# Optimization experiments

Measured on AMD Instinct MI355X. Metric: run time of the kernel, lower is better.

Reference implementation:

```python
import jax, jax.numpy as jnp
import numpy as np

B, C, H, W = 64, 64, 56, 56
MID = 2 * C  # two output nodes concatenated
EPS = 1e-5


def _conv1x1(x, w):
    # x: [B,C,H,W], w: [O,C] (1x1 conv kernel squeezed)
    return jnp.einsum('bchw,oc->bohw', x, w)


def _bn(x, g, b, m, v):
    # eval-mode BatchNorm2d with running stats
    sc = g * jax.lax.rsqrt(v + EPS)
    return x * sc[None, :, None, None] + (b - m * sc)[None, :, None, None]


def _maxpool3(x):
    # MaxPool2d(kernel=3, stride=1, padding=1)
    return jax.lax.reduce_window(x, -jnp.inf, jax.lax.max,
                                 (1, 1, 3, 3), (1, 1, 1, 1),
                                 [(0, 0), (0, 0), (1, 1), (1, 1)])


def _avgpool3(x):
    # AvgPool2d(kernel=3, stride=1, padding=1), count_include_pad=True -> /9
    s = jax.lax.reduce_window(x, 0.0, jax.lax.add,
                              (1, 1, 3, 3), (1, 1, 1, 1),
                              [(0, 0), (0, 0), (1, 1), (1, 1)])
    return s * (1.0 / 9.0)


def setup_inputs() -> dict:
    key = jax.random.key(0)
    ks = jax.random.split(key, 11)
    x = jax.random.normal(ks[0], (B, C, H, W), dtype=jnp.float32)
    w1 = jax.random.normal(ks[1], (C, C), dtype=jnp.float32) * 0.1
    w2 = jax.random.normal(ks[2], (C, MID), dtype=jnp.float32) * 0.1
    bn1_g = 1.0 + 0.1 * jax.random.normal(ks[3], (C,), dtype=jnp.float32)
    bn1_b = 0.1 * jax.random.normal(ks[4], (C,), dtype=jnp.float32)
    bn1_m = 0.1 * jax.random.normal(ks[5], (C,), dtype=jnp.float32)
    bn1_v = jax.random.uniform(ks[6], (C,), minval=0.5, maxval=1.5, dtype=jnp.float32)
    bn2_g = 1.0 + 0.1 * jax.random.normal(ks[7], (C,), dtype=jnp.float32)
    bn2_b = 0.1 * jax.random.normal(ks[8], (C,), dtype=jnp.float32)
    bn2_m = 0.1 * jax.random.normal(ks[9], (C,), dtype=jnp.float32)
    bn2_v = jax.random.uniform(ks[10], (C,), minval=0.5, maxval=1.5, dtype=jnp.float32)
    return dict(x=x, w1=w1, w2=w2,
                bn1_g=bn1_g, bn1_b=bn1_b, bn1_m=bn1_m, bn1_v=bn1_v,
                bn2_g=bn2_g, bn2_b=bn2_b, bn2_m=bn2_m, bn2_v=bn2_v)


def reference(x, w1, w2, bn1_g, bn1_b, bn1_m, bn1_v, bn2_g, bn2_b, bn2_m, bn2_v):
    # DAG g = [[[0,1],[1,2]], [[4,3],[3]], [[5,3],[3,100]], [[4,3],[100]]]
    # topoSort order: [0, 2, 1, 3]; output nodes (ordered): [2, 3]
    node0 = jax.nn.relu(_bn(_conv1x1(x, w1), bn1_g, bn1_b, bn1_m, bn1_v))
    node1 = _maxpool3(node0)            # op type 4, pred {0}
    node2 = _avgpool3(node0)            # op type 5, pred {0}
    node3 = _maxpool3(node1) + _maxpool3(node2)  # op type 4, preds {1,2}, summed
    cat = jnp.concatenate([node2, node3], axis=1)  # [B, 2C, H, W]
    out = jax.nn.relu(_bn(_conv1x1(cat, w2), bn2_g, bn2_b, bn2_m, bn2_v))
    return out
```

## Files before the change

kernel.cpp:

```cpp
#include <hip/hip_runtime.h>
#include <cstddef>

#define EPS 1e-5f
static constexpr int Bn = 64, Cn = 64, Hn = 56, Wn = 56, HWn = Hn * Wn;
static constexpr int XS = 65;
static constexpr int RB = 8;
static constexpr int NBAND = 7;
static constexpr int SLAB = 3600;

typedef __attribute__((ext_vector_type(8))) short short8;
typedef __attribute__((ext_vector_type(8))) unsigned short ushort8;
typedef __attribute__((ext_vector_type(4))) unsigned short ushort4v;
typedef __attribute__((ext_vector_type(4))) float floatx4;
typedef __attribute__((ext_vector_type(4))) unsigned int uintx4;
typedef __attribute__((ext_vector_type(2))) unsigned int uintx2;

__device__ __forceinline__ unsigned pack_rne(float a, float b) {
    unsigned ua = __float_as_uint(a), ub = __float_as_uint(b);
    ua = ua + 0x7fffu + ((ua >> 16) & 1u);
    ub = ub + 0x7fffu + ((ub >> 16) & 1u);
    return __builtin_amdgcn_perm(ub, ua, 0x07060302);
}
__device__ __forceinline__ unsigned pack_trunc(float a, float b) {
    return __builtin_amdgcn_perm(__float_as_uint(b), __float_as_uint(a), 0x07060302);
}
__device__ __forceinline__ ushort8 pmax(ushort8 a, ushort8 b) {
    return __builtin_elementwise_max(a, b);
}
__device__ __forceinline__ uintx2 pmax2(uintx2 a, uintx2 b) {
    ushort4v r = __builtin_elementwise_max(*(ushort4v*)&a, *(ushort4v*)&b);
    return *(uintx2*)&r;
}
__device__ __forceinline__ float bf_lo(unsigned u) { return __uint_as_float(u << 16); }
__device__ __forceinline__ float bf_hi(unsigned u) { return __uint_as_float(u & 0xffff0000u); }


__global__ __launch_bounds__(256) void k1_conv1(
    const float* __restrict__ x, const float* __restrict__ w1,
    const float* __restrict__ bg, const float* __restrict__ bb,
    const float* __restrict__ bm, const float* __restrict__ bv,
    unsigned short* __restrict__ node0)
{
    __shared__ float xs[2][64 * XS];
    __shared__ float scs[64], shs[64];
    const int tid = threadIdx.x;
    if (tid < 64) {
        float sc = bg[tid] * rsqrtf(bv[tid] + EPS);
        scs[tid] = sc;
        shs[tid] = bb[tid] - bm[tid] * sc;
    }
    __syncthreads();
    const int lane = tid & 63;
    const int wv   = tid >> 6;
    const int m    = lane & 15;
    const int quad = lane >> 4;
    const int qoff = quad * 8;

    short8 afr[4][2];
    float shv[16];
    #pragma unroll
    for (int t = 0; t < 4; ++t) {
        const float sc = scs[t * 16 + m];
        #pragma unroll
        for (int kk = 0; kk < 2; ++kk) {
            const float* wp = w1 + (t * 16 + m) * 64 + kk * 32 + qoff;
            floatx4 f0 = *(const floatx4*)wp;
            floatx4 f1 = *(const floatx4*)(wp + 4);
            uintx4 u;
            u.x = pack_rne(f0[0] * sc, f0[1] * sc);
            u.y = pack_rne(f0[2] * sc, f0[3] * sc);
            u.z = pack_rne(f1[0] * sc, f1[1] * sc);
            u.w = pack_rne(f1[2] * sc, f1[3] * sc);
            afr[t][kk] = *(short8*)&u;
        }
        #pragma unroll
        for (int i = 0; i < 4; ++i) shv[t * 4 + i] = shs[t * 16 + quad * 4 + i];
    }

    floatx4 stg[4];
    auto ldtile = [&](int tt) {
        const int P = blockIdx.x * 256 + tt * 64;
        const int b = P / HWn, p0 = P - b * HWn;
        #pragma unroll
        for (int q = 0; q < 4; ++q) {
            int idx = q * 256 + tid;
            int c = idx >> 4, f = idx & 15;
            stg[q] = *(const floatx4*)(x + (size_t)(b * 64 + c) * HWn + p0 + f * 4);
        }
    };
    auto sttile = [&](int buf) {
        #pragma unroll
        for (int q = 0; q < 4; ++q) {
            int idx = q * 256 + tid;
            int c = idx >> 4, f = idx & 15;
            #pragma unroll
            for (int k = 0; k < 4; ++k)
                xs[buf][(f * 4 + k) * XS + c] = stg[q][k];
        }
    };

    ldtile(0);
    sttile(0);

    #pragma unroll
    for (int tt = 0; tt < 4; ++tt) {
        __syncthreads();
        if (tt < 3) ldtile(tt + 1);

        const int P = blockIdx.x * 256 + tt * 64;
        const int b = P / HWn, p0 = P - b * HWn;
        const float* xr = &xs[tt & 1][(wv * 16 + m) * XS];

        floatx4 acc[4];
        #pragma unroll
        for (int t = 0; t < 4; ++t) acc[t] = (floatx4){0.f, 0.f, 0.f, 0.f};

        #pragma unroll
        for (int kk = 0; kk < 2; ++kk) {
            float f[8];
            #pragma unroll
            for (int j = 0; j < 8; ++j) f[j] = xr[kk * 32 + qoff + j];
            uintx4 u;
            u.x = pack_trunc(f[0], f[1]);
            u.y = pack_trunc(f[2], f[3]);
            u.z = pack_trunc(f[4], f[5]);
            u.w = pack_trunc(f[6], f[7]);
            short8 bfr = *(short8*)&u;
            #pragma unroll
            for (int t = 0; t < 4; ++t)
                acc[t] = __builtin_amdgcn_mfma_f32_16x16x32_bf16(afr[t][kk], bfr, acc[t], 0, 0, 0);
        }

        const int chunkbase = (quad >> 1);
        const int j0 = (quad & 1) * 4;
        #pragma unroll
        for (int t = 0; t < 4; ++t) {
            float v0 = acc[t][0] + shv[t * 4 + 0]; v0 = v0 > 0.f ? v0 : 0.f;
            float v1 = acc[t][1] + shv[t * 4 + 1]; v1 = v1 > 0.f ? v1 : 0.f;
            float v2 = acc[t][2] + shv[t * 4 + 2]; v2 = v2 > 0.f ? v2 : 0.f;
            float v3 = acc[t][3] + shv[t * 4 + 3]; v3 = v3 > 0.f ? v3 : 0.f;
            uintx2 st;
            st.x = pack_rne(v0, v1);
            st.y = pack_rne(v2, v3);
            int chunk = t * 2 + chunkbase;
            *(uintx2*)(node0 + ((size_t)(b * 8 + chunk) * HWn + p0 + wv * 16 + m) * 8 + j0) = st;
        }

        if (tt < 3) sttile((tt + 1) & 1);
    }
}

__global__ __launch_bounds__(1024, 4) void k23_fused(
    const unsigned short* __restrict__ node0,
    const float* __restrict__ w2,
    const float* __restrict__ bg, const float* __restrict__ bb,
    const float* __restrict__ bm, const float* __restrict__ bv,
    float* __restrict__ out)
{
    __shared__ __align__(16) unsigned short catl[16 * SLAB];
    const int tid = threadIdx.x;
    const int lane = tid & 63;
    const int wv = tid >> 6;

    const int bid = blockIdx.x;
    const int xcd = bid & 7;
    const int jj = bid >> 3;
    const int b = xcd * 8 + jj / NBAND;
    const int band = jj % NBAND;
    const int lo = band * RB;

    {
        const int chunk = wv >> 1;
        const int c0 = (wv & 1) * 28;
        const int local = lane >> 1;
        const int col = c0 - 2 + local;
        const int jh = lane & 1;
        const unsigned short* base = node0 + ((size_t)(b * 8 + chunk) * HWn) * 8 + jh * 4;

        const uintx2 zz = (uintx2){0u, 0u};
        auto loadrow = [&](int r) -> uintx2 {
            if (((unsigned)col >= (unsigned)Wn) | ((unsigned)r >= (unsigned)Hn)) return zz;
            return *(const uintx2*)(base + (size_t)(r * Wn + col) * 8);
        };

        float hs1[4], hs2[4];
        #pragma unroll
        for (int c = 0; c < 4; ++c) hs1[c] = hs2[c] = 0.f;
        uintx2 h5a = zz, h5b = zz, h5c = zz, h5d = zz, nh1 = zz, nh2 = zz;

        uintx2 cur = loadrow(lo - 2);
        uintx2 nxt = loadrow(lo - 1);

        unsigned short* cav = catl + (size_t)(chunk * 2) * SLAB + jh * 4;
        unsigned short* cmx = cav + SLAB;
        const bool stcol = (local >= 2) & (local <= 29);

        #pragma unroll
        for (int i = 0; i < RB + 4; ++i) {
            const int r = lo - 2 + i;
            uintx2 nx2 = (i < RB + 2) ? loadrow(r + 2) : zz;

            uintx2 D0, D1, D3, D4;
            #pragma unroll
            for (int w = 0; w < 2; ++w) {
                unsigned u = cur[w];
                D1[w] = __shfl_up(u, 2);
                D0[w] = __shfl_up(u, 4);
                D3[w] = __shfl_down(u, 2);
                D4[w] = __shfl_down(u, 4);
            }

            uintx2 hm5 = pmax2(pmax2(pmax2(D0, D1), pmax2(cur, D3)), D4);
            uintx2 m5 = pmax2(pmax2(pmax2(h5a, h5b), pmax2(h5c, h5d)), hm5);
            h5a = h5b; h5b = h5c; h5c = h5d; h5d = hm5;

            float a2[4];
            #pragma unroll
            for (int w = 0; w < 2; ++w) {
                float s0 = bf_lo(D1[w]) + bf_lo(cur[w]) + bf_lo(D3[w]);
                float s1 = bf_hi(D1[w]) + bf_hi(cur[w]) + bf_hi(D3[w]);
                a2[w * 2 + 0] = (hs2[w * 2 + 0] + hs1[w * 2 + 0] + s0) * (1.f / 9.f);
                a2[w * 2 + 1] = (hs2[w * 2 + 1] + hs1[w * 2 + 1] + s1) * (1.f / 9.f);
                hs2[w * 2 + 0] = hs1[w * 2 + 0]; hs1[w * 2 + 0] = s0;
                hs2[w * 2 + 1] = hs1[w * 2 + 1]; hs1[w * 2 + 1] = s1;
            }
            uintx2 ap;
            ap.x = pack_rne(a2[0], a2[1]);
            ap.y = pack_rne(a2[2], a2[3]);

            uintx2 al, ar;
            #pragma unroll
            for (int w = 0; w < 2; ++w) {
                al[w] = __shfl_up(ap[w], 2);
                ar[w] = __shfl_down(ap[w], 2);
            }
            uintx2 nh = pmax2(pmax2(al, ap), ar);
            uintx2 m3 = pmax2(pmax2(nh2, nh1), nh);
            nh2 = nh1; nh1 = nh;

            const int r2 = r - 1, r3 = r - 2;
            if (stcol && i >= 3 && i <= RB + 2)
                *(uintx2*)(cav + (size_t)((r2 - lo) * Wn + col) * 8) = ap;
            if (stcol && i >= 4) {
                uintx2 st;
                st.x = pack_rne(bf_lo(m5.x) + bf_lo(m3.x), bf_hi(m5.x) + bf_hi(m3.x));
                st.y = pack_rne(bf_lo(m5.y) + bf_lo(m3.y), bf_hi(m5.y) + bf_hi(m3.y));
                *(uintx2*)(cmx + (size_t)((r3 - lo) * Wn + col) * 8) = st;
            }
            cur = nxt; nxt = nx2;
        }
    }

    const int m16 = lane & 15;
    const int q = lane >> 4;
    const int t = wv & 3;
    const int e = wv >> 2;
    short8 afr[4];
    #pragma unroll
    for (int cp = 0; cp < 4; ++cp) {
        const int c = 2 * cp + (q >> 1);
        const int chb = ((q & 1) ? 64 : 0) + 8 * c;
        const float* wp = w2 + (size_t)(t * 16 + m16) * 128 + chb;
        floatx4 f0 = *(const floatx4*)wp;
        floatx4 f1 = *(const floatx4*)(wp + 4);
        uintx4 u;
        u.x = pack_rne(f0[0], f0[1]);
        u.y = pack_rne(f0[2], f0[3]);
        u.z = pack_rne(f1[0], f1[1]);
        u.w = pack_rne(f1[2], f1[3]);
        afr[cp] = *(short8*)&u;
    }
    const int oc0 = t * 16 + q * 4;
    floatx4 g4 = *(const floatx4*)(bg + oc0);
    floatx4 bb4 = *(const floatx4*)(bb + oc0);
    floatx4 mm4 = *(const floatx4*)(bm + oc0);
    floatx4 vv4 = *(const floatx4*)(bv + oc0);
    float sc[4], sh[4];
    #pragma unroll
    for (int r = 0; r < 4; ++r) {
        sc[r] = g4[r] * rsqrtf(vv4[r] + EPS);
        sh[r] = bb4[r] - mm4[r] * sc[r];
    }
    __syncthreads();

    floatx4 acc[7];
    #pragma unroll
    for (int i = 0; i < 7; ++i) acc[i] = (floatx4){0.f, 0.f, 0.f, 0.f};

    #pragma unroll
    for (int cp = 0; cp < 4; ++cp) {
        #pragma unroll
        for (int i = 0; i < 7; ++i) {
            const int px = (e * 7 + i) * 16 + m16;
            short8 bfr = *(const short8*)(catl + (size_t)(4 * cp + q) * SLAB + (size_t)px * 8);
            acc[i] = __builtin_amdgcn_mfma_f32_16x16x32_bf16(afr[cp], bfr, acc[i], 0, 0, 0);
        }
    }

    float* ob = out + (size_t)(b * 64 + oc0) * HWn + lo * Wn;
    #pragma unroll
    for (int i = 0; i < 7; ++i) {
        const int px = (e * 7 + i) * 16 + m16;
        #pragma unroll
        for (int r = 0; r < 4; ++r) {
            float v = fmaf(acc[i][r], sc[r], sh[r]);
            ob[(size_t)r * HWn + px] = v > 0.f ? v : 0.f;
        }
    }
}

extern "C" void kernel_launch(void* const* d_in, const int* in_sizes, int n_in,
                              void* d_out, int out_size, void* d_ws, size_t ws_size,
                              hipStream_t stream)
{
    const float* x   = (const float*)d_in[0];
    const float* w1  = (const float*)d_in[1];
    const float* w2  = (const float*)d_in[2];
    const float* b1g = (const float*)d_in[3];
    const float* b1b = (const float*)d_in[4];
    const float* b1m = (const float*)d_in[5];
    const float* b1v = (const float*)d_in[6];
    const float* b2g = (const float*)d_in[7];
    const float* b2b = (const float*)d_in[8];
    const float* b2m = (const float*)d_in[9];
    const float* b2v = (const float*)d_in[10];

    float* out = (float*)d_out;
    unsigned short* node0 = (unsigned short*)d_ws;

    k1_conv1<<<dim3(784), dim3(256), 0, stream>>>(x, w1, b1g, b1b, b1m, b1v, node0);
    k23_fused<<<dim3(Bn * NBAND), dim3(1024), 0, stream>>>(node0, w2, b2g, b2b, b2m, b2v, out);
}
```

Before: 146.6 us.

## Rewrite conv1 with 32x32x16 MFMA and direct global loads, drop LDS staging

The first 1x1 conv kernel no longer stages a transposed x tile through shared memory with double buffering. Each wave now loads its 32 pixels x 64 channels straight from global memory into registers and runs 32x32x16 bf16 MFMAs for two 32-channel output halves. Launch bounds now request 4 blocks per CU. This removes the LDS writes and reads and the per-tile barriers, but the global loads become strided per channel: each lane reads one float per channel row, coalesced across lanes only within a 32-pixel span.

```diff
diff --git a/kernel.cpp b/kernel.cpp
--- a/kernel.cpp
+++ b/kernel.cpp
@@ -3,7 +3,6 @@
 
 #define EPS 1e-5f
 static constexpr int Bn = 64, Cn = 64, Hn = 56, Wn = 56, HWn = Hn * Wn;
-static constexpr int XS = 65;
 static constexpr int RB = 8;
 static constexpr int NBAND = 7;
 static constexpr int SLAB = 3600;
@@ -12,6 +11,7 @@
 typedef __attribute__((ext_vector_type(8))) unsigned short ushort8;
 typedef __attribute__((ext_vector_type(4))) unsigned short ushort4v;
 typedef __attribute__((ext_vector_type(4))) float floatx4;
+typedef __attribute__((ext_vector_type(16))) float floatx16;
 typedef __attribute__((ext_vector_type(4))) unsigned int uintx4;
 typedef __attribute__((ext_vector_type(2))) unsigned int uintx2;
 
@@ -24,9 +24,6 @@
 __device__ __forceinline__ unsigned pack_trunc(float a, float b) {
     return __builtin_amdgcn_perm(__float_as_uint(b), __float_as_uint(a), 0x07060302);
 }
-__device__ __forceinline__ ushort8 pmax(ushort8 a, ushort8 b) {
-    return __builtin_elementwise_max(a, b);
-}
 __device__ __forceinline__ uintx2 pmax2(uintx2 a, uintx2 b) {
     ushort4v r = __builtin_elementwise_max(*(ushort4v*)&a, *(ushort4v*)&b);
     return *(uintx2*)&r;
@@ -35,13 +32,12 @@
 __device__ __forceinline__ float bf_hi(unsigned u) { return __uint_as_float(u & 0xffff0000u); }
 
 
-__global__ __launch_bounds__(256) void k1_conv1(
+__global__ __launch_bounds__(256, 4) void k1_conv1(
     const float* __restrict__ x, const float* __restrict__ w1,
     const float* __restrict__ bg, const float* __restrict__ bb,
     const float* __restrict__ bm, const float* __restrict__ bv,
     unsigned short* __restrict__ node0)
 {
-    __shared__ float xs[2][64 * XS];
     __shared__ float scs[64], shs[64];
     const int tid = threadIdx.x;
     if (tid < 64) {
@@ -52,101 +48,80 @@
     __syncthreads();
     const int lane = tid & 63;
     const int wv   = tid >> 6;
-    const int m    = lane & 15;
-    const int quad = lane >> 4;
-    const int qoff = quad * 8;
-
-    short8 afr[4][2];
-    float shv[16];
-    #pragma unroll
-    for (int t = 0; t < 4; ++t) {
-        const float sc = scs[t * 16 + m];
-        #pragma unroll
-        for (int kk = 0; kk < 2; ++kk) {
-            const float* wp = w1 + (t * 16 + m) * 64 + kk * 32 + qoff;
-            floatx4 f0 = *(const floatx4*)wp;
-            floatx4 f1 = *(const floatx4*)(wp + 4);
+    const int n    = lane & 31;
+    const int h    = lane >> 5;
+
+    short8 afr0[4], afr1[4];
+    {
+        const float s0 = scs[n], s1 = scs[32 + n];
+        #pragma unroll
+        for (int kt = 0; kt < 4; ++kt) {
+            const float* wp0 = w1 + (size_t)n * 64 + kt * 16 + h * 8;
+            floatx4 f0 = *(const floatx4*)wp0;
+            floatx4 f1 = *(const floatx4*)(wp0 + 4);
             uintx4 u;
-            u.x = pack_rne(f0[0] * sc, f0[1] * sc);
-            u.y = pack_rne(f0[2] * sc, f0[3] * sc);
-            u.z = pack_rne(f1[0] * sc, f1[1] * sc);
-            u.w = pack_rne(f1[2] * sc, f1[3] * sc);
-            afr[t][kk] = *(short8*)&u;
-        }
-        #pragma unroll
-        for (int i = 0; i < 4; ++i) shv[t * 4 + i] = shs[t * 16 + quad * 4 + i];
-    }
-
-    floatx4 stg[4];
-    auto ldtile = [&](int tt) {
-        const int P = blockIdx.x * 256 + tt * 64;
+            u.x = pack_rne(f0[0] * s0, f0[1] * s0);
+            u.y = pack_rne(f0[2] * s0, f0[3] * s0);
+            u.z = pack_rne(f1[0] * s0, f1[1] * s0);
+            u.w = pack_rne(f1[2] * s0, f1[3] * s0);
+            afr0[kt] = *(short8*)&u;
+            const float* wp1 = wp0 + 32 * 64;
+            floatx4 g0 = *(const floatx4*)wp1;
+            floatx4 g1 = *(const floatx4*)(wp1 + 4);
+            uintx4 v;
+            v.x = pack_rne(g0[0] * s1, g0[1] * s1);
+            v.y = pack_rne(g0[2] * s1, g0[3] * s1);
+            v.z = pack_rne(g1[0] * s1, g1[1] * s1);
+            v.w = pack_rne(g1[2] * s1, g1[3] * s1);
+            afr1[kt] = *(short8*)&v;
+        }
+    }
+
+    #pragma unroll
+    for (int s = 0; s < 2; ++s) {
+        const int P = blockIdx.x * 256 + (wv * 2 + s) * 32;
         const int b = P / HWn, p0 = P - b * HWn;
-        #pragma unroll
-        for (int q = 0; q < 4; ++q) {
-            int idx = q * 256 + tid;
-            int c = idx >> 4, f = idx & 15;
-            stg[q] = *(const floatx4*)(x + (size_t)(b * 64 + c) * HWn + p0 + f * 4);
-        }
-    };
-    auto sttile = [&](int buf) {
-        #pragma unroll
-        for (int q = 0; q < 4; ++q) {
-            int idx = q * 256 + tid;
-            int c = idx >> 4, f = idx & 15;
-            #pragma unroll
-            for (int k = 0; k < 4; ++k)
-                xs[buf][(f * 4 + k) * XS + c] = stg[q][k];
-        }
-    };
-
-    ldtile(0);
-    sttile(0);
-
-    #pragma unroll
-    for (int tt = 0; tt < 4; ++tt) {
-        __syncthreads();
-        if (tt < 3) ldtile(tt + 1);
-
-        const int P = blockIdx.x * 256 + tt * 64;
-        const int b = P / HWn, p0 = P - b * HWn;
-        const float* xr = &xs[tt & 1][(wv * 16 + m) * XS];
-
-        floatx4 acc[4];
-        #pragma unroll
-        for (int t = 0; t < 4; ++t) acc[t] = (floatx4){0.f, 0.f, 0.f, 0.f};
-
-        #pragma unroll
-        for (int kk = 0; kk < 2; ++kk) {
-            float f[8];
-            #pragma unroll
-            for (int j = 0; j < 8; ++j) f[j] = xr[kk * 32 + qoff + j];
+        const float* xb = x + (size_t)b * 64 * HWn + p0 + n;
+
+        float f[4][8];
+        #pragma unroll
+        for (int kt = 0; kt < 4; ++kt)
+            #pragma unroll
+            for (int j = 0; j < 8; ++j)
+                f[kt][j] = xb[(size_t)(kt * 16 + h * 8 + j) * HWn];
+
+        floatx16 acc0, acc1;
+        #pragma unroll
+        for (int i = 0; i < 16; ++i) { acc0[i] = 0.f; acc1[i] = 0.f; }
+
+        #pragma unroll
+        for (int kt = 0; kt < 4; ++kt) {
             uintx4 u;
-            u.x = pack_trunc(f[0], f[1]);
-            u.y = pack_trunc(f[2], f[3]);
-            u.z = pack_trunc(f[4], f[5]);
-            u.w = pack_trunc(f[6], f[7]);
+            u.x = pack_trunc(f[kt][0], f[kt][1]);
+            u.y = pack_trunc(f[kt][2], f[kt][3]);
+            u.z = pack_trunc(f[kt][4], f[kt][5]);
+            u.w = pack_trunc(f[kt][6], f[kt][7]);
             short8 bfr = *(short8*)&u;
-            #pragma unroll
-            for (int t = 0; t < 4; ++t)
-                acc[t] = __builtin_amdgcn_mfma_f32_16x16x32_bf16(afr[t][kk], bfr, acc[t], 0, 0, 0);
-        }
-
-        const int chunkbase = (quad >> 1);
-        const int j0 = (quad & 1) * 4;
-        #pragma unroll
-        for (int t = 0; t < 4; ++t) {
-            float v0 = acc[t][0] + shv[t * 4 + 0]; v0 = v0 > 0.f ? v0 : 0.f;
-            float v1 = acc[t][1] + shv[t * 4 + 1]; v1 = v1 > 0.f ? v1 : 0.f;
-            float v2 = acc[t][2] + shv[t * 4 + 2]; v2 = v2 > 0.f ? v2 : 0.f;
-            float v3 = acc[t][3] + shv[t * 4 + 3]; v3 = v3 > 0.f ? v3 : 0.f;
-            uintx2 st;
-            st.x = pack_rne(v0, v1);
-            st.y = pack_rne(v2, v3);
-            int chunk = t * 2 + chunkbase;
-            *(uintx2*)(node0 + ((size_t)(b * 8 + chunk) * HWn + p0 + wv * 16 + m) * 8 + j0) = st;
-        }
-
-        if (tt < 3) sttile((tt + 1) & 1);
+            acc0 = __builtin_amdgcn_mfma_f32_32x32x16_bf16(afr0[kt], bfr, acc0, 0, 0, 0);
+            acc1 = __builtin_amdgcn_mfma_f32_32x32x16_bf16(afr1[kt], bfr, acc1, 0, 0, 0);
+        }
+
+        #pragma unroll
+        for (int oct = 0; oct < 2; ++oct) {
+            #pragma unroll
+            for (int g = 0; g < 4; ++g) {
+                floatx4 sh4 = *(const floatx4*)&shs[oct * 32 + g * 8 + h * 4];
+                float v0 = (oct ? acc1[g * 4 + 0] : acc0[g * 4 + 0]) + sh4[0]; v0 = v0 > 0.f ? v0 : 0.f;
+                float v1 = (oct ? acc1[g * 4 + 1] : acc0[g * 4 + 1]) + sh4[1]; v1 = v1 > 0.f ? v1 : 0.f;
+                float v2 = (oct ? acc1[g * 4 + 2] : acc0[g * 4 + 2]) + sh4[2]; v2 = v2 > 0.f ? v2 : 0.f;
+                float v3 = (oct ? acc1[g * 4 + 3] : acc0[g * 4 + 3]) + sh4[3]; v3 = v3 > 0.f ? v3 : 0.f;
+                uintx2 st;
+                st.x = pack_rne(v0, v1);
+                st.y = pack_rne(v2, v3);
+                const int chunk = oct * 4 + g;
+                *(uintx2*)(node0 + ((size_t)(b * 8 + chunk) * HWn + p0 + n) * 8 + h * 4) = st;
+            }
+        }
     }
 }
 
```

Result: no change. 148.2 us (+1.1%).
